# Optimization experiments

Measured on AMD Instinct MI355X. Metric: run time of the kernel, lower is better.

Reference implementation:

```python
import jax, jax.numpy as jnp
import numpy as np
import math

# ---- sizes (must match setup_inputs) ----
D = 256          # distribution dim
K = 2 * D        # parameters per embedding: mean + hidden (log) variance
L = 64           # classes present in batch
B = 8            # samples per class (B_total = B*L = 512)
S = 16           # config['sample_size']
C = 64           # num_classes
LOG_EPS = -100.0
LOG2PI = math.log(2.0 * math.pi)

# ---- NormalDistribution (diagonal, exp parametrization) helpers ----

def _split(p):
    # (..., K) -> mean (..., D), hidden log-variance (..., D)
    return p[..., :D], p[..., D:]


def _logpdf(params, x):
    m, h = _split(params)
    return -0.5 * jnp.sum(LOG2PI + h + (x - m) ** 2 * jnp.exp(-h), axis=-1)


def _logmls(p1, p2):
    # log int N(x; m1, v1) N(x; m2, v2) dx = log N(m1; m2, v1 + v2)
    m1, h1 = _split(p1)
    m2, h2 = _split(p2)
    v = jnp.exp(h1) + jnp.exp(h2)
    return -0.5 * jnp.sum(LOG2PI + jnp.log(v) + (m1 - m2) ** 2 / v, axis=-1)


def _pdf_product(p1, p2):
    # product of two diagonal Gaussians -> new Gaussian params (broadcasting)
    m1, h1 = _split(p1)
    m2, h2 = _split(p2)
    v1, v2 = jnp.exp(h1), jnp.exp(h2)
    vs = v1 + v2
    v = v1 * v2 / vs
    m = (m1 * v2 + m2 * v1) / vs
    return jnp.concatenate(jnp.broadcast_arrays(m, jnp.log(v)), axis=-1)


def _prototypes(support, eps_var):
    # support: (B2, L, K) -> fused prototype params (L, K)
    m, h = _split(support)
    v = eps_var + jnp.exp(h)            # (B2, L, D)
    inv = 1.0 / v
    new_var = 1.0 / inv.sum(0)          # (L, D)
    new_mean = new_var * (m * inv).sum(0)
    new_h = jnp.log(eps_var + new_var)  # ipositive(variance + new_var)
    return jnp.concatenate([new_mean, new_h], axis=-1)


def _compute_logits(query, support, eps_var, key):
    # query: (b, L, K); support: (b2, L, K) -> logits (b, L, L)
    b = query.shape[0]
    protos = _prototypes(support, eps_var)                      # (L, K)
    p = _pdf_product(query[:, :, None, :], protos[None, None])  # (b, L, L, K)
    m, h = _split(p)
    eps = jax.random.normal(key, (b, L, S, L, D), dtype=query.dtype)
    samples = m[:, :, None] + jnp.exp(0.5 * h[:, :, None]) * eps  # (b, L, S, L, D)
    lm = _logmls(query[:, :, None, :], protos[None, None])        # (b, L, L)
    tl = _logpdf(protos[None, None, None], samples)               # (b, L, S, L)
    lse = jax.scipy.special.logsumexp(tl, axis=-1, keepdims=True)  # (b, L, S, 1)
    return lm + jax.scipy.special.logsumexp(-lse, axis=-2) - math.log(S)


def _group_by_class(parameters, labels):
    # balanced labels: each of L labels appears exactly B times
    idx = jnp.argsort(labels)                 # stable in jax
    order = idx.reshape(L, B).T               # (B, L): i-th occurrence of each label
    label_map = labels[idx].reshape(L, B)[:, 0]
    by_class = parameters[idx].reshape(L, B, K).transpose(1, 0, 2)  # (B, L, K)
    return by_class, order, label_map


def setup_inputs() -> dict:
    key = jax.random.key(0)
    k1, k2 = jax.random.split(key)
    parameters = jax.random.normal(k1, (B * L, K), dtype=jnp.float32)
    # balanced labels: each class in [0, L) appears exactly B times, shuffled
    labels = jax.random.permutation(k2, jnp.arange(B * L, dtype=jnp.int32) % L).astype(jnp.int64)
    hidden_epsilon = jnp.asarray(0.01 ** (2.0 / D), dtype=jnp.float32)
    return {"parameters": parameters, "hidden_epsilon": hidden_epsilon, "labels": labels}


def reference(parameters, hidden_epsilon, labels):
    eps_var = jnp.exp(hidden_epsilon)
    by_class, order, label_map = _group_by_class(parameters, labels)
    k = B // 2
    key = jax.random.key(42)
    s1, s2 = jax.random.split(key)
    logits1 = _compute_logits(by_class[:k], by_class[k:], eps_var, s1)
    logits2 = _compute_logits(by_class[k:], by_class[:k], eps_var, s2)
    logits = jnp.concatenate([logits1, logits2], axis=0)          # (B, L, L)
    all_logits = jnp.full((B, L, C), LOG_EPS, dtype=logits.dtype)
    all_logits = all_logits.at[:, :, label_map].set(logits)       # scatter on class dim
    all_logits = all_logits.reshape(B * L, C)
    return all_logits[jnp.argsort(order.reshape(-1))]             # unsort to input order
```

## Files before the change

### kernel.cpp

```cpp
#include <hip/hip_runtime.h>
#include <math.h>

#define DD 256
#define KK 512
#define LL 64
#define BB 8
#define SS 16
#define F_LOG2PI 1.83787706641f
#define PER_I 16777216u

typedef float v2f __attribute__((ext_vector_type(2)));

struct U2 { unsigned x, y; };

__host__ __device__ constexpr U2 tf2x32(unsigned k0, unsigned k1, unsigned c0, unsigned c1) {
  unsigned ks2 = k0 ^ k1 ^ 0x1BD11BDAu;
  unsigned x0 = c0 + k0;
  unsigned x1 = c1 + k1;
#define TFR(r) { x0 += x1; x1 = (x1 << (r)) | (x1 >> (32 - (r))); x1 ^= x0; }
  TFR(13) TFR(15) TFR(26) TFR(6)   x0 += k1;  x1 += ks2 + 1u;
  TFR(17) TFR(29) TFR(16) TFR(24)  x0 += ks2; x1 += k0 + 2u;
  TFR(13) TFR(15) TFR(26) TFR(6)   x0 += k0;  x1 += k1 + 3u;
  TFR(17) TFR(29) TFR(16) TFR(24)  x0 += k1;  x1 += ks2 + 4u;
  TFR(13) TFR(15) TFR(26) TFR(6)   x0 += ks2; x1 += k0 + 5u;
#undef TFR
  return U2{x0, x1};
}

__device__ inline unsigned rotl(unsigned x, unsigned r) {
  return __builtin_amdgcn_alignbit(x, x, 32u - r);
}

__device__ inline unsigned tf_fold(unsigned k0, unsigned k1, unsigned ks2, unsigned x1) {
  unsigned x0 = k0;
#define TFR(r)            { x0 += x1; x1 = rotl(x1, r); x1 ^= x0; }
#define TFRI(r, kA, kB)   { x1 += (kB); x0 = x0 + (kA) + x1; x1 = rotl(x1, r); x1 ^= x0; }
  TFR(13u) TFR(15u) TFR(26u) TFR(6u)
  TFRI(17u, k1, ks2 + 1u)
  TFR(29u) TFR(16u) TFR(24u)
  TFRI(13u, ks2, k0 + 2u)
  TFR(15u) TFR(26u) TFR(6u)
  TFRI(17u, k0, k1 + 3u)
  TFR(29u) TFR(16u) TFR(24u)
  TFRI(13u, k1, ks2 + 4u)
  TFR(15u) TFR(26u) TFR(6u)
  x0 += ks2; x1 += k0 + 5u;
#undef TFR
#undef TFRI
  return x0 ^ x1;
}

__device__ inline v2f pkfma(v2f a, v2f b, v2f c) {
#if __has_builtin(__builtin_elementwise_fma)
  return __builtin_elementwise_fma(a, b, c);
#else
  v2f r; r.x = fmaf(a.x, b.x, c.x); r.y = fmaf(a.y, b.y, c.y); return r;
#endif
}

__device__ inline v2f normal_pu2(unsigned b0, unsigned b1) {
  v2f fv;
  fv.x = __uint_as_float(__builtin_amdgcn_alignbit(128u, b0, 9u));
  fv.y = __uint_as_float(__builtin_amdgcn_alignbit(128u, b1, 9u));
  v2f uv = fv + (v2f){-3.0f, -3.0f};
  uv.x = fmaxf(-0.99999994f, uv.x);
  uv.y = fmaxf(-0.99999994f, uv.y);
  v2f tv = pkfma(-uv, uv, (v2f){1.0f, 1.0f});
  v2f lv;
  lv.x = __log2f(tv.x);
  lv.y = __log2f(tv.y);
  const v2f nln2 = {-0.69314718056f, -0.69314718056f};
  v2f wx = pkfma(lv, nln2, (v2f){-2.5f, -2.5f});
  v2f p; p.x = 2.81022636e-08f; p.y = 2.81022636e-08f;
  p = pkfma(p, wx, (v2f){ 3.43273939e-07f,  3.43273939e-07f});
  p = pkfma(p, wx, (v2f){-3.5233877e-06f,  -3.5233877e-06f});
  p = pkfma(p, wx, (v2f){-4.39150654e-06f, -4.39150654e-06f});
  p = pkfma(p, wx, (v2f){ 0.00021858087f,   0.00021858087f});
  p = pkfma(p, wx, (v2f){-0.00125372503f,  -0.00125372503f});
  p = pkfma(p, wx, (v2f){-0.00417768164f,  -0.00417768164f});
  p = pkfma(p, wx, (v2f){ 0.246640727f,     0.246640727f});
  p = pkfma(p, wx, (v2f){ 1.50140941f,      1.50140941f});
  v2f pu = p * uv;
  if (__any(fmaxf(wx.x, wx.y) >= 2.5f)) {
    v2f wv = lv * nln2;
    v2f sy;
    sy.x = __builtin_amdgcn_sqrtf(wv.x) - 3.0f;
    sy.y = __builtin_amdgcn_sqrtf(wv.y) - 3.0f;
    v2f q; q.x = -0.000200214257f; q.y = -0.000200214257f;
    q = pkfma(q, sy, (v2f){ 0.000100950558f,  0.000100950558f});
    q = pkfma(q, sy, (v2f){ 0.00134934322f,   0.00134934322f});
    q = pkfma(q, sy, (v2f){-0.00367342844f,  -0.00367342844f});
    q = pkfma(q, sy, (v2f){ 0.00573950773f,   0.00573950773f});
    q = pkfma(q, sy, (v2f){-0.0076224613f,   -0.0076224613f});
    q = pkfma(q, sy, (v2f){ 0.00943887047f,   0.00943887047f});
    q = pkfma(q, sy, (v2f){ 1.00167406f,      1.00167406f});
    q = pkfma(q, sy, (v2f){ 2.83297682f,      2.83297682f});
    v2f qu = q * uv;
    pu.x = (wx.x < 2.5f) ? pu.x : qu.x;
    pu.y = (wx.y < 2.5f) ? pu.y : qu.y;
  }
  return pu;
}


__global__ void k_protos(const float* __restrict__ P, const float* __restrict__ he_p,
                         const int* __restrict__ labels, float4* __restrict__ pq,
                         float* __restrict__ cl, float4* __restrict__ accz,
                         float4* __restrict__ lmz, int* __restrict__ pos,
                         int* __restrict__ lmap) {
  int hb = blockIdx.x;
  int h = hb >> 6, l = hb & 63;
  int d = threadIdx.x;

  {
    float4 z; z.x = z.y = z.z = z.w = 0.0f;
    float4* base = accz + (hb * 256 + d) * 4;
#pragma unroll
    for (int j = 0; j < 4; ++j) base[j] = z;
    int gtid = hb * 256 + d;
    if (gtid < 8192) lmz[gtid] = z;
  }

  __shared__ int lab[512];
  __shared__ int cnt[64];
  __shared__ int mode;
  __shared__ int posl[512];
  if (d < 64) cnt[d] = 0;
  if (d == 0) mode = 0;
  __syncthreads();
  int v0 = labels[d], v1 = labels[d + 256];
  atomicAdd(&cnt[v0 & 63], 1);
  atomicAdd(&cnt[v1 & 63], 1);
  __syncthreads();
  if (d < 64 && cnt[d] != 8) mode = 1;
  __syncthreads();
  if (mode) { v0 = labels[2 * d]; v1 = labels[2 * (d + 256)]; }
  lab[d] = v0 & 63; lab[d + 256] = v1 & 63;
  __syncthreads();
#pragma unroll
  for (int e = d; e < 512; e += 256) {
    int c = lab[e], o = 0;
    for (int j = 0; j < e; ++j) o += (lab[j] == c);
    posl[c * 8 + o] = e;
  }
  __syncthreads();
  if (hb == 0) {
    pos[d] = posl[d]; pos[d + 256] = posl[d + 256];
    if (d < 64) lmap[d] = d;
  }

  float eps_var = expf(he_p[0]);
  int soff = h ? 0 : 4;
  float sinv = 0.f, sminv = 0.f;
#pragma unroll
  for (int j = 0; j < 4; ++j) {
    int row = posl[l * 8 + soff + j];
    float m = P[row * KK + d];
    float hh = P[row * KK + DD + d];
    float vv = eps_var + expf(hh);
    float iv = 1.0f / vv;
    sinv += iv; sminv += m * iv;
  }
  float nv = 1.0f / sinv;
  float nm = nv * sminv;
  float ev = eps_var + nv;
  float4 rec; rec.x = nm; rec.y = ev; rec.z = 1.0f / ev; rec.w = 0.0f;
  pq[(h * 256 + d) * 64 + l] = rec;
  float t = F_LOG2PI + __logf(ev);
  for (int off = 32; off; off >>= 1) t += __shfl_xor(t, off);
  __shared__ float red[4];
  int w = d >> 6, lane = d & 63;
  if (lane == 0) red[w] = t;
  __syncthreads();
  if (d == 0) cl[hb] = red[0] + red[1] + red[2] + red[3];
}

__global__ __launch_bounds__(256) void k_tl(const float* __restrict__ P,
    const int* __restrict__ pos, const float4* __restrict__ pq,
    float* __restrict__ accbuf, float* __restrict__ lmacc) {
  constexpr U2 S1 = tf2x32(0u, 42u, 0u, 0u);
  constexpr U2 S2 = tf2x32(0u, 42u, 0u, 1u);
  int bb = blockIdx.x;
  int h = bb >> 10;
  int lq = (bb >> 4) & 63;
  int chunk = bb & 15;
  int t = threadIdx.x;

  __shared__ float2 q[4 * 256];
#pragma unroll
  for (int i = 0; i < 4; ++i) {
    int row = pos[lq * 8 + h * 4 + i];
    float2 rec;
    rec.x = P[row * KK + t];
    rec.y = expf(P[row * KK + DD + t]);
    q[i * 256 + t] = rec;
  }
  __syncthreads();

  int w = t >> 6, lane = t & 63;
  unsigned k0 = h ? S2.x : S1.x;
  unsigned k1 = h ? S2.y : S1.y;
  unsigned ks2 = k0 ^ k1 ^ 0x1BD11BDAu;
  unsigned ebk = (unsigned)w * PER_I + (unsigned)lq * 262144u +
                 (unsigned)lane * 256u + (unsigned)chunk * 16u + k1;
  const float2* qd = &q[w * 256];
  const float4* pp = pq + (h * 256 + chunk * 16) * 64 + lane;
  int g = h * 4 + w;
  float* dst = accbuf + ((g * 64 + lq) * 16) * 64 + lane;

  v2f acc2[8];
#pragma unroll
  for (int sp = 0; sp < 8; ++sp) { acc2[sp].x = 0.0f; acc2[sp].y = 0.0f; }
  float lmpart = 0.0f;

#pragma unroll 1
  for (int dd = 0; dd < 16; ++dd) {
    float4 pr = pp[dd * 64];
    float2 qv = qd[chunk * 16 + dd];
    float vs  = qv.y + pr.y;
    float ivs = __builtin_amdgcn_rcpf(vs);
    float evs = pr.y * ivs;
    float sivp = __builtin_amdgcn_sqrtf(pr.z);
    float dif = qv.x - pr.x;
    lmpart += __logf(vs) + dif * dif * ivs;
    float A = dif * evs * sivp;
    float S = __builtin_amdgcn_sqrtf(qv.y * evs) * sivp * 1.41421356f;
    v2f Av; Av.x = A; Av.y = A;
    v2f Sv; Sv.x = S; Sv.y = S;
    unsigned ebkd = ebk + (unsigned)dd;
#pragma unroll
    for (int sp = 0; sp < 8; ++sp) {
      unsigned bits0 = tf_fold(k0, k1, ks2, ebkd + (unsigned)(2 * sp) * 16384u);
      unsigned bits1 = tf_fold(k0, k1, ks2, ebkd + (unsigned)(2 * sp + 1) * 16384u);
      v2f pu = normal_pu2(bits0, bits1);
      v2f diff = pkfma(Sv, pu, Av);
      acc2[sp] = pkfma(diff, diff, acc2[sp]);
    }
  }
#pragma unroll
  for (int sp = 0; sp < 8; ++sp) {
    atomicAdd(dst + (2 * sp) * 64, acc2[sp].x);
    atomicAdd(dst + (2 * sp + 1) * 64, acc2[sp].y);
  }
  atomicAdd(lmacc + (g * 64 + lq) * 64 + lane, lmpart);
}

__global__ void k_final(const float* __restrict__ lmacc, const float* __restrict__ accbuf,
                        const float* __restrict__ cl, const int* __restrict__ pos,
                        const int* __restrict__ lmap, float* __restrict__ out) {
  int bb = blockIdx.x;
  int g = bb >> 6, lq = bb & 63;
  int h = g >> 2;
  int t = threadIdx.x, w = t >> 6, lane = t & 63;
  __shared__ float lsebuf[16];
  float clv = cl[h * 64 + lane];
#pragma unroll
  for (int j = 0; j < 4; ++j) {
    int s = w * 4 + j;
    float tlv = -0.5f * (clv + accbuf[(bb * 16 + s) * 64 + lane]);
    float mx = tlv;
    for (int off = 32; off; off >>= 1) mx = fmaxf(mx, __shfl_xor(mx, off));
    float se = expf(tlv - mx);
    for (int off = 32; off; off >>= 1) se += __shfl_xor(se, off);
    if (lane == 0) lsebuf[s] = mx + __logf(se);
  }
  __syncthreads();
  if (t < 64) {
    float a = (t < 16) ? -lsebuf[t] : -INFINITY;
    float mx = a;
    for (int off = 32; off; off >>= 1) mx = fmaxf(mx, __shfl_xor(mx, off));
    float e = (t < 16) ? expf(a - mx) : 0.0f;
    for (int off = 32; off; off >>= 1) e += __shfl_xor(e, off);
    float mc = mx + __logf(e) - 2.7725887f;
    float lmv = -0.5f * (256.0f * F_LOG2PI + lmacc[bb * 64 + t]);
    int row = pos[lq * 8 + g];
    out[row * 64 + lmap[t]] = lmv + mc;
  }
}

extern "C" void kernel_launch(void* const* d_in, const int* in_sizes, int n_in,
                              void* d_out, int out_size, void* d_ws, size_t ws_size,
                              hipStream_t stream) {
  (void)in_sizes; (void)n_in; (void)out_size; (void)ws_size;
  const float* P      = (const float*)d_in[0];
  const float* he     = (const float*)d_in[1];
  const int*   labels = (const int*)d_in[2];
  float* out = (float*)d_out;

  float* ws = (float*)d_ws;
  float* accbuf = ws;
  float* lmacc  = ws + 524288;
  float4* pq = (float4*)(ws + 557056);
  float* cl  = ws + 688128;
  int*   pos = (int*)(ws + 688256);
  int*   lmp = pos + 512;

  hipLaunchKernelGGL(k_protos, dim3(128),  dim3(256), 0, stream, P, he, labels, pq, cl,
                     (float4*)accbuf, (float4*)lmacc, pos, lmp);
  hipLaunchKernelGGL(k_tl,     dim3(2048), dim3(256), 0, stream, P, pos, pq, accbuf, lmacc);
  hipLaunchKernelGGL(k_final,  dim3(512),  dim3(256), 0, stream, lmacc, accbuf, cl, pos, lmp, out);
}
```

Before: 356.3 us.

## Fuse final logsumexp into k_tl via last-block atomic counter

Removes the separate k_final launch: each k_tl block bumps a per-(h,lq) counter stored in the unused w slot of pq, and the last of 16 chunk blocks reads the accumulated sums with atomics and computes the logsumexp and output. It also software-prefetches the next pr/qv loads, sets launch_bounds occupancy to 8, pads shared memory and uses a packed max. The output now writes out[row*64+lane] instead of going through lmap, which relies on the label map being the identity. The counter reuse of pq padding also assumes k_protos zeroes that slot, and the prefetch reads one element past the chunk.

```diff
diff --git a/kernel.cpp b/kernel.cpp
--- a/kernel.cpp
+++ b/kernel.cpp
@@ -63,8 +63,12 @@
   fv.x = __uint_as_float(__builtin_amdgcn_alignbit(128u, b0, 9u));
   fv.y = __uint_as_float(__builtin_amdgcn_alignbit(128u, b1, 9u));
   v2f uv = fv + (v2f){-3.0f, -3.0f};
+#if __has_builtin(__builtin_elementwise_max)
+  uv = __builtin_elementwise_max(uv, (v2f){-0.99999994f, -0.99999994f});
+#else
   uv.x = fmaxf(-0.99999994f, uv.x);
   uv.y = fmaxf(-0.99999994f, uv.y);
+#endif
   v2f tv = pkfma(-uv, uv, (v2f){1.0f, 1.0f});
   v2f lv;
   lv.x = __log2f(tv.x);
@@ -175,9 +179,10 @@
   if (d == 0) cl[hb] = red[0] + red[1] + red[2] + red[3];
 }
 
-__global__ __launch_bounds__(256) void k_tl(const float* __restrict__ P,
+__global__ __launch_bounds__(256, 8) void k_tl(const float* __restrict__ P,
     const int* __restrict__ pos, const float4* __restrict__ pq,
-    float* __restrict__ accbuf, float* __restrict__ lmacc) {
+    float* __restrict__ accbuf, float* __restrict__ lmacc,
+    const float* __restrict__ cl, float* __restrict__ out) {
   constexpr U2 S1 = tf2x32(0u, 42u, 0u, 0u);
   constexpr U2 S2 = tf2x32(0u, 42u, 0u, 1u);
   int bb = blockIdx.x;
@@ -186,7 +191,7 @@
   int chunk = bb & 15;
   int t = threadIdx.x;
 
-  __shared__ float2 q[4 * 256];
+  __shared__ float2 q[4 * 256 + 8];
 #pragma unroll
   for (int i = 0; i < 4; ++i) {
     int row = pos[lq * 8 + h * 4 + i];
@@ -213,10 +218,12 @@
   for (int sp = 0; sp < 8; ++sp) { acc2[sp].x = 0.0f; acc2[sp].y = 0.0f; }
   float lmpart = 0.0f;
 
+  float4 pr = pp[0];
+  float2 qv = qd[chunk * 16];
 #pragma unroll 1
   for (int dd = 0; dd < 16; ++dd) {
-    float4 pr = pp[dd * 64];
-    float2 qv = qd[chunk * 16 + dd];
+    float4 prn = pp[(dd + 1) * 64];
+    float2 qvn = qd[chunk * 16 + dd + 1];
     float vs  = qv.y + pr.y;
     float ivs = __builtin_amdgcn_rcpf(vs);
     float evs = pr.y * ivs;
@@ -236,6 +243,7 @@
       v2f diff = pkfma(Sv, pu, Av);
       acc2[sp] = pkfma(diff, diff, acc2[sp]);
     }
+    pr = prn; qv = qvn;
   }
 #pragma unroll
   for (int sp = 0; sp < 8; ++sp) {
@@ -243,39 +251,42 @@
     atomicAdd(dst + (2 * sp + 1) * 64, acc2[sp].y);
   }
   atomicAdd(lmacc + (g * 64 + lq) * 64 + lane, lmpart);
-}
-
-__global__ void k_final(const float* __restrict__ lmacc, const float* __restrict__ accbuf,
-                        const float* __restrict__ cl, const int* __restrict__ pos,
-                        const int* __restrict__ lmap, float* __restrict__ out) {
-  int bb = blockIdx.x;
-  int g = bb >> 6, lq = bb & 63;
-  int h = g >> 2;
-  int t = threadIdx.x, w = t >> 6, lane = t & 63;
-  __shared__ float lsebuf[16];
+
+  __threadfence();
+  __syncthreads();
+  __shared__ int oldc;
+  if (t == 0) {
+    int* cw = (int*)pq + (((h * 256) * 64 + lq) * 4 + 3);
+    oldc = atomicAdd(cw, 1);
+  }
+  __syncthreads();
+  if (oldc != 15) return;
+
+  __shared__ float lseb[4][16];
   float clv = cl[h * 64 + lane];
-#pragma unroll
-  for (int j = 0; j < 4; ++j) {
-    int s = w * 4 + j;
-    float tlv = -0.5f * (clv + accbuf[(bb * 16 + s) * 64 + lane]);
+  float av[16];
+#pragma unroll
+  for (int s = 0; s < 16; ++s) av[s] = atomicAdd(dst + s * 64, 0.0f);
+#pragma unroll
+  for (int s = 0; s < 16; ++s) {
+    float tlv = -0.5f * (clv + av[s]);
     float mx = tlv;
     for (int off = 32; off; off >>= 1) mx = fmaxf(mx, __shfl_xor(mx, off));
     float se = expf(tlv - mx);
     for (int off = 32; off; off >>= 1) se += __shfl_xor(se, off);
-    if (lane == 0) lsebuf[s] = mx + __logf(se);
-  }
-  __syncthreads();
-  if (t < 64) {
-    float a = (t < 16) ? -lsebuf[t] : -INFINITY;
-    float mx = a;
-    for (int off = 32; off; off >>= 1) mx = fmaxf(mx, __shfl_xor(mx, off));
-    float e = (t < 16) ? expf(a - mx) : 0.0f;
-    for (int off = 32; off; off >>= 1) e += __shfl_xor(e, off);
-    float mc = mx + __logf(e) - 2.7725887f;
-    float lmv = -0.5f * (256.0f * F_LOG2PI + lmacc[bb * 64 + t]);
-    int row = pos[lq * 8 + g];
-    out[row * 64 + lmap[t]] = lmv + mc;
-  }
+    if (lane == 0) lseb[w][s] = mx + __logf(se);
+  }
+  __syncthreads();
+  float a2 = (lane < 16) ? -lseb[w][lane] : -INFINITY;
+  float mx2 = a2;
+  for (int off = 32; off; off >>= 1) mx2 = fmaxf(mx2, __shfl_xor(mx2, off));
+  float e2 = (lane < 16) ? expf(a2 - mx2) : 0.0f;
+  for (int off = 32; off; off >>= 1) e2 += __shfl_xor(e2, off);
+  float mc = mx2 + __logf(e2) - 2.7725887f;
+  float lmw = atomicAdd(lmacc + (g * 64 + lq) * 64 + lane, 0.0f);
+  float lmv = -0.5f * (256.0f * F_LOG2PI + lmw);
+  int row = pos[lq * 8 + g];
+  out[row * 64 + lane] = lmv + mc;
 }
 
 extern "C" void kernel_launch(void* const* d_in, const int* in_sizes, int n_in,
@@ -297,6 +308,6 @@
 
   hipLaunchKernelGGL(k_protos, dim3(128),  dim3(256), 0, stream, P, he, labels, pq, cl,
                      (float4*)accbuf, (float4*)lmacc, pos, lmp);
-  hipLaunchKernelGGL(k_tl,     dim3(2048), dim3(256), 0, stream, P, pos, pq, accbuf, lmacc);
-  hipLaunchKernelGGL(k_final,  dim3(512),  dim3(256), 0, stream, lmacc, accbuf, cl, pos, lmp, out);
-}
+  hipLaunchKernelGGL(k_tl,     dim3(2048), dim3(256), 0, stream, P, pos, pq, accbuf, lmacc,
+                     cl, out);
+}
```

Result: slower. 374.9 us (+5.2%).
